# Kernel tuning notes

Hardware: AMD Instinct MI355X
Metric: run time of the kernel (lower is better)

The kernel has to match this reference:

```python
import jax, jax.numpy as jnp
import numpy as np

P = 512
H, W = 256, 256
TANFOVX = 0.5
TANFOVY = 0.5
NEAR = 0.2  # frustum near-plane cull as in 3DGS preprocess
COV_BLUR = 0.3  # low-pass filter added to 2D covariance diagonal (3DGS)
ALPHA_MIN = 1.0 / 255.0
ALPHA_MAX = 0.99


def quat_to_rotmat(q):
    # q: [P,4] normalized (r, x, y, z) -> [P,3,3]
    r, x, y, z = q[:, 0], q[:, 1], q[:, 2], q[:, 3]
    R = jnp.stack([
        1 - 2 * (y * y + z * z), 2 * (x * y - r * z), 2 * (x * z + r * y),
        2 * (x * y + r * z), 1 - 2 * (x * x + z * z), 2 * (y * z - r * x),
        2 * (x * z - r * y), 2 * (y * z + r * x), 1 - 2 * (x * x + y * y),
    ], axis=-1)
    return R.reshape(-1, 3, 3)


def setup_inputs() -> dict:
    key = jax.random.key(0)
    ks = jax.random.split(key, 6)
    # Gaussians in front of a camera at the origin looking down +z.
    xy = jax.random.uniform(ks[0], (P, 2), minval=-2.0, maxval=2.0)
    z = jax.random.uniform(ks[1], (P, 1), minval=2.0, maxval=6.0)
    means3D = jnp.concatenate([xy, z], axis=-1).astype(jnp.float32)
    opacities = jax.random.normal(ks[2], (P, 1), dtype=jnp.float32)  # logits
    scales = (jnp.log(0.05) + 0.3 * jax.random.normal(ks[3], (P, 3))).astype(jnp.float32)  # log-scales
    rotations = jax.random.normal(ks[4], (P, 4), dtype=jnp.float32)  # raw quats
    colors_precomp = jax.random.uniform(ks[5], (P, 3), dtype=jnp.float32)
    viewmatrix = jnp.eye(4, dtype=jnp.float32)
    n, f = NEAR, 100.0
    proj = np.zeros((4, 4), np.float32)
    proj[0, 0] = 1.0 / TANFOVX
    proj[1, 1] = 1.0 / TANFOVY
    proj[2, 2] = f / (f - n)
    proj[2, 3] = -f * n / (f - n)
    proj[3, 2] = 1.0
    projmatrix = jnp.asarray(proj)  # full (proj @ view) since view = I
    campos = jnp.zeros(3, jnp.float32)
    bg = jnp.zeros(3, jnp.float32)
    return dict(means3D=means3D, opacities=opacities, scales=scales,
                rotations=rotations, colors_precomp=colors_precomp,
                viewmatrix=viewmatrix, projmatrix=projmatrix, campos=campos, bg=bg)


def reference(means3D, opacities, scales, rotations, colors_precomp,
              viewmatrix, projmatrix, campos, bg):
    # --- activations applied by the autograd Function forward ---
    opa = jax.nn.sigmoid(opacities[:, 0])                      # [P]
    s = jnp.exp(scales)                                        # [P,3]
    q = rotations / jnp.clip(jnp.linalg.norm(rotations, axis=-1, keepdims=True), 1e-12)
    R = quat_to_rotmat(q)                                      # [P,3,3]
    # 3D covariance: cov = (R S)(R S)^T
    L = R * s[:, None, :]
    cov3D = jnp.einsum('pij,pkj->pik', L, L)                   # [P,3,3]
    # --- camera-space transform ---
    t = means3D @ viewmatrix[:3, :3].T + viewmatrix[:3, 3]     # [P,3]
    tx, ty, tz = t[:, 0], t[:, 1], t[:, 2]
    valid = tz > NEAR
    tzc = jnp.where(valid, tz, 1.0)
    limx, limy = 1.3 * TANFOVX, 1.3 * TANFOVY
    txz = jnp.clip(tx / tzc, -limx, limx) * tzc
    tyz = jnp.clip(ty / tzc, -limy, limy) * tzc
    fx = W / (2.0 * TANFOVX)
    fy = H / (2.0 * TANFOVY)
    # --- EWA splatting: 2D covariance = J W cov3D W^T J^T ---
    zeros = jnp.zeros_like(tzc)
    J = jnp.stack([
        jnp.stack([fx / tzc, zeros, -fx * txz / (tzc * tzc)], axis=-1),
        jnp.stack([zeros, fy / tzc, -fy * tyz / (tzc * tzc)], axis=-1),
    ], axis=-2)                                                # [P,2,3]
    T = jnp.einsum('pij,jk->pik', J, viewmatrix[:3, :3])       # [P,2,3]
    cov2D = jnp.einsum('pij,pjk,plk->pil', T, cov3D, T)        # [P,2,2]
    cov2D = cov2D + COV_BLUR * jnp.eye(2, dtype=cov2D.dtype)
    det = cov2D[:, 0, 0] * cov2D[:, 1, 1] - cov2D[:, 0, 1] ** 2
    det = jnp.where(det == 0.0, 1.0, det)
    conA = cov2D[:, 1, 1] / det
    conB = -cov2D[:, 0, 1] / det
    conC = cov2D[:, 0, 0] / det
    # --- projection to pixel coordinates ---
    ph = jnp.concatenate([means3D, jnp.ones((means3D.shape[0], 1), means3D.dtype)], -1) @ projmatrix.T
    pw = 1.0 / (ph[:, 3] + 1e-7)
    pix_x = ((ph[:, 0] * pw + 1.0) * W - 1.0) * 0.5            # [P]
    pix_y = ((ph[:, 1] * pw + 1.0) * H - 1.0) * 0.5
    # --- global front-to-back depth sort (stand-in for tile binning + per-tile sort) ---
    depth = jnp.where(valid, tz, jnp.inf)
    order = jnp.argsort(depth)
    opa_s = opa[order]
    conA_s, conB_s, conC_s = conA[order], conB[order], conC[order]
    px_s, py_s = pix_x[order], pix_y[order]
    valid_s = valid[order]
    col_s = colors_precomp[order]
    # --- dense alpha compositing over all pixels ---
    xg = jnp.arange(W, dtype=jnp.float32)
    yg = jnp.arange(H, dtype=jnp.float32)
    dx = px_s[:, None, None] - xg[None, None, :]               # [P,1,W]
    dy = py_s[:, None, None] - yg[None, :, None]               # [P,H,1]
    power = (-0.5 * (conA_s[:, None, None] * dx * dx + conC_s[:, None, None] * dy * dy)
             - conB_s[:, None, None] * dx * dy)                # [P,H,W]
    alpha = jnp.minimum(ALPHA_MAX, opa_s[:, None, None] * jnp.exp(power))
    alpha = jnp.where((power > 0.0) | (alpha < ALPHA_MIN) | (~valid_s[:, None, None]), 0.0, alpha)
    Tcum = jnp.cumprod(1.0 - alpha, axis=0)                    # [P,H,W]
    Tprev = jnp.concatenate([jnp.ones((1, H, W), alpha.dtype), Tcum[:-1]], axis=0)
    wgt = alpha * Tprev                                        # per-Gaussian compositing weight
    out_color = jnp.einsum('phw,pc->hwc', wgt, col_s) + Tcum[-1][..., None] * bg  # [H,W,3]
    return out_color
```

## Files before the change

### kernel.cpp

```cpp
#include <hip/hip_runtime.h>
#include <math.h>

#define PCOUNT 512
#define IMG_W 256
#define IMG_H 256
#define TANX 0.5f
#define TANY 0.5f
#define NEARP 0.2f
#define BLUR 0.3f
#define AMIN (1.0f/255.0f)
#define AMAX 0.99f

__global__ __launch_bounds__(256) void fused_raster_kernel(
    const float* __restrict__ means, const float* __restrict__ opac,
    const float* __restrict__ scales, const float* __restrict__ rots,
    const float* __restrict__ cols, const float* __restrict__ vm,
    const float* __restrict__ pm, const float* __restrict__ bg,
    float* __restrict__ out)
{
    __shared__ float s_params[PCOUNT * 12];
    __shared__ float s_depth[PCOUNT];
    __shared__ unsigned short s_order[PCOUNT];
    __shared__ int s_wcnt[4];
    __shared__ int s_base;

    int t = threadIdx.x;
    int wave = t >> 6, lane = t & 63;
    int tileX = blockIdx.x & 15, tileY = blockIdx.x >> 4;
    float tx0 = (float)(tileX << 4), tx1 = tx0 + 15.0f;
    float ty0 = (float)(tileY << 4), ty1 = ty0 + 15.0f;

    if (t == 0) s_base = 0;
    __syncthreads();

    #pragma unroll
    for (int c = 0; c < 2; ++c) {
        int g = c * 256 + t;

        float mx = means[3*g], my = means[3*g+1], mz = means[3*g+2];
        float o = 1.0f / (1.0f + __expf(-opac[g]));
        float sx = __expf(scales[3*g]), sy = __expf(scales[3*g+1]), sz = __expf(scales[3*g+2]);

        float qr = rots[4*g], qx = rots[4*g+1], qy = rots[4*g+2], qz = rots[4*g+3];
        float qn = fmaxf(sqrtf(qr*qr + qx*qx + qy*qy + qz*qz), 1e-12f);
        float qi = 1.0f/qn;
        qr *= qi; qx *= qi; qy *= qi; qz *= qi;

        float R00 = 1.0f-2.0f*(qy*qy+qz*qz), R01 = 2.0f*(qx*qy - qr*qz), R02 = 2.0f*(qx*qz + qr*qy);
        float R10 = 2.0f*(qx*qy + qr*qz), R11 = 1.0f-2.0f*(qx*qx+qz*qz), R12 = 2.0f*(qy*qz - qr*qx);
        float R20 = 2.0f*(qx*qz - qr*qy), R21 = 2.0f*(qy*qz + qr*qx), R22 = 1.0f-2.0f*(qx*qx+qy*qy);

        float s0 = sx*sx, s1 = sy*sy, s2 = sz*sz;
        float c00 = R00*R00*s0 + R01*R01*s1 + R02*R02*s2;
        float c01 = R00*R10*s0 + R01*R11*s1 + R02*R12*s2;
        float c02 = R00*R20*s0 + R01*R21*s1 + R02*R22*s2;
        float c11 = R10*R10*s0 + R11*R11*s1 + R12*R12*s2;
        float c12 = R10*R20*s0 + R11*R21*s1 + R12*R22*s2;
        float c22 = R20*R20*s0 + R21*R21*s1 + R22*R22*s2;

        float tx = vm[0]*mx + vm[1]*my + vm[2]*mz + vm[3];
        float ty = vm[4]*mx + vm[5]*my + vm[6]*mz + vm[7];
        float tz = vm[8]*mx + vm[9]*my + vm[10]*mz + vm[11];
        bool valid = tz > NEARP;
        float tzc = valid ? tz : 1.0f;

        float limx = 1.3f*TANX, limy = 1.3f*TANY;
        float txz = fminf(fmaxf(tx/tzc, -limx), limx)*tzc;
        float tyz = fminf(fmaxf(ty/tzc, -limy), limy)*tzc;

        float fx = (float)IMG_W/(2.0f*TANX), fy = (float)IMG_H/(2.0f*TANY);
        float J00 = fx/tzc, J02 = -fx*txz/(tzc*tzc);
        float J11 = fy/tzc, J12 = -fy*tyz/(tzc*tzc);

        float T00 = J00*vm[0] + J02*vm[8];
        float T01 = J00*vm[1] + J02*vm[9];
        float T02 = J00*vm[2] + J02*vm[10];
        float T10 = J11*vm[4] + J12*vm[8];
        float T11 = J11*vm[5] + J12*vm[9];
        float T12 = J11*vm[6] + J12*vm[10];

        float M00 = T00*c00 + T01*c01 + T02*c02;
        float M01 = T00*c01 + T01*c11 + T02*c12;
        float M02 = T00*c02 + T01*c12 + T02*c22;
        float M10 = T10*c00 + T11*c01 + T12*c02;
        float M11 = T10*c01 + T11*c11 + T12*c12;
        float M12 = T10*c02 + T11*c12 + T12*c22;
        float v00 = M00*T00 + M01*T01 + M02*T02 + BLUR;
        float v01 = M00*T10 + M01*T11 + M02*T12;
        float v11 = M10*T10 + M11*T11 + M12*T12 + BLUR;

        float det = v00*v11 - v01*v01;
        det = (det == 0.0f) ? 1.0f : det;
        float idet = 1.0f/det;
        float conA = v11*idet, conB = -v01*idet, conC = v00*idet;

        float ph0 = pm[0]*mx + pm[1]*my + pm[2]*mz + pm[3];
        float ph1 = pm[4]*mx + pm[5]*my + pm[6]*mz + pm[7];
        float ph3 = pm[12]*mx + pm[13]*my + pm[14]*mz + pm[15];
        float pw = 1.0f/(ph3 + 1e-7f);
        float px = ((ph0*pw + 1.0f)*(float)IMG_W - 1.0f)*0.5f;
        float py = ((ph1*pw + 1.0f)*(float)IMG_H - 1.0f)*0.5f;

        float opa_eff = valid ? o : 0.0f;

        bool hit = false;
        float oa = opa_eff * 255.0f;
        if (oa > 1.0f) {
            float r2 = 2.0f * __logf(oa);
            float dxm = sqrtf(r2 * v00) + 1.0f;
            float dym = sqrtf(r2 * v11) + 1.0f;
            hit = (px - dxm <= tx1) & (px + dxm >= tx0) &
                  (py - dym <= ty1) & (py + dym >= ty0);
        }

        unsigned long long m = __ballot(hit);
        int rnk = __popcll(m & ((1ull << lane) - 1ull));
        if (lane == 0) s_wcnt[wave] = __popcll(m);
        __syncthreads();
        int off = s_base;
        for (int w = 0; w < wave; ++w) off += s_wcnt[w];
        if (hit) {
            int slot = off + rnk;
            float* p = &s_params[slot * 12];
            p[0] = conA; p[1] = conB; p[2] = conC; p[3] = px;
            p[4] = py;   p[5] = opa_eff;
            p[6] = cols[3*g]; p[7] = cols[3*g+1]; p[8] = cols[3*g+2];
            s_depth[slot] = tz;
        }
        __syncthreads();
        if (t == 0) s_base += s_wcnt[0] + s_wcnt[1] + s_wcnt[2] + s_wcnt[3];
        __syncthreads();
    }
    int total = s_base;

    if (t < total) {
        float dk = s_depth[t];
        int rank = 0;
        for (int j = 0; j < total; ++j) {
            float dj = s_depth[j];
            rank += (int)((dj < dk) || (dj == dk && j < t));
        }
        s_order[rank] = (unsigned short)t;
    }
    __syncthreads();

    int lx = t & 15, ly = t >> 4;
    float fxp = tx0 + (float)lx, fyp = ty0 + (float)ly;

    float T = 1.0f, cr = 0.0f, cg = 0.0f, cb = 0.0f;
    for (int i = 0; i < total; ++i) {
        int k = s_order[i];
        const float* p = &s_params[k * 12];
        float4 p0 = *(const float4*)(p);
        float4 p1 = *(const float4*)(p + 4);
        float pb  = p[8];
        float dx = p0.w - fxp;
        float dy = p1.x - fyp;
        float power = -0.5f*(p0.x*dx*dx + p0.z*dy*dy) - p0.y*dx*dy;
        if (power <= 0.0f) {
            float al = p1.y * __expf(power);
            if (al >= AMIN) {
                al = fminf(al, AMAX);
                float w = al * T;
                cr += w * p1.z;
                cg += w * p1.w;
                cb += w * pb;
                T *= (1.0f - al);
            }
        }
    }

    int x = (tileX << 4) + lx, y = (tileY << 4) + ly;
    int o = (y*IMG_W + x)*3;
    out[o+0] = cr + T*bg[0];
    out[o+1] = cg + T*bg[1];
    out[o+2] = cb + T*bg[2];
}

extern "C" void kernel_launch(void* const* d_in, const int* in_sizes, int n_in,
                              void* d_out, int out_size, void* d_ws, size_t ws_size,
                              hipStream_t stream) {
    const float* means  = (const float*)d_in[0];
    const float* opac   = (const float*)d_in[1];
    const float* scales = (const float*)d_in[2];
    const float* rots   = (const float*)d_in[3];
    const float* cols   = (const float*)d_in[4];
    const float* vm     = (const float*)d_in[5];
    const float* pm     = (const float*)d_in[6];
    const float* bg     = (const float*)d_in[8];

    fused_raster_kernel<<<256, 256, 0, stream>>>(
        means, opac, scales, rots, cols, vm, pm, bg, (float*)d_out);
}
```

Measured before the change: 13.24 us.

## Split per-pixel compositing across four depth segments with 1024-thread blocks

Raises the block size to 1024 threads. Each Gaussian is preprocessed by its own thread instead of looping over two chunks, which drops the extra barriers. The depth-sorted list is split into four contiguous segments, and each segment is composited by a separate group of 256 threads. The partial (color, transmittance) results are then combined in order through shared memory. This shortens the serial per-pixel loop, at the cost of losing early-termination benefits, an extra reduction step, and more shared memory per block.

Result: faster. 10.63 us (-19.7%).

```diff
diff --git a/kernel.cpp b/kernel.cpp
--- a/kernel.cpp
+++ b/kernel.cpp
@@ -11,7 +11,7 @@
 #define AMIN (1.0f/255.0f)
 #define AMAX 0.99f
 
-__global__ __launch_bounds__(256) void fused_raster_kernel(
+__global__ __launch_bounds__(1024) void fused_raster_kernel(
     const float* __restrict__ means, const float* __restrict__ opac,
     const float* __restrict__ scales, const float* __restrict__ rots,
     const float* __restrict__ cols, const float* __restrict__ vm,
@@ -21,8 +21,9 @@
     __shared__ float s_params[PCOUNT * 12];
     __shared__ float s_depth[PCOUNT];
     __shared__ unsigned short s_order[PCOUNT];
-    __shared__ int s_wcnt[4];
-    __shared__ int s_base;
+    __shared__ float4 s_part[4][256];
+    __shared__ int s_wcnt[16];
+    __shared__ int s_total;
 
     int t = threadIdx.x;
     int wave = t >> 6, lane = t & 63;
@@ -30,13 +31,10 @@
     float tx0 = (float)(tileX << 4), tx1 = tx0 + 15.0f;
     float ty0 = (float)(tileY << 4), ty1 = ty0 + 15.0f;
 
-    if (t == 0) s_base = 0;
-    __syncthreads();
-
-    #pragma unroll
-    for (int c = 0; c < 2; ++c) {
-        int g = c * 256 + t;
-
+    bool hit = false;
+    float conA = 0, conB = 0, conC = 0, px = 0, py = 0, opa_eff = 0, tz = 0;
+    int g = t;
+    if (t < PCOUNT) {
         float mx = means[3*g], my = means[3*g+1], mz = means[3*g+2];
         float o = 1.0f / (1.0f + __expf(-opac[g]));
         float sx = __expf(scales[3*g]), sy = __expf(scales[3*g+1]), sz = __expf(scales[3*g+2]);
@@ -58,15 +56,15 @@
         float c12 = R10*R20*s0 + R11*R21*s1 + R12*R22*s2;
         float c22 = R20*R20*s0 + R21*R21*s1 + R22*R22*s2;
 
-        float tx = vm[0]*mx + vm[1]*my + vm[2]*mz + vm[3];
-        float ty = vm[4]*mx + vm[5]*my + vm[6]*mz + vm[7];
-        float tz = vm[8]*mx + vm[9]*my + vm[10]*mz + vm[11];
+        float tvx = vm[0]*mx + vm[1]*my + vm[2]*mz + vm[3];
+        float tvy = vm[4]*mx + vm[5]*my + vm[6]*mz + vm[7];
+        tz = vm[8]*mx + vm[9]*my + vm[10]*mz + vm[11];
         bool valid = tz > NEARP;
         float tzc = valid ? tz : 1.0f;
 
         float limx = 1.3f*TANX, limy = 1.3f*TANY;
-        float txz = fminf(fmaxf(tx/tzc, -limx), limx)*tzc;
-        float tyz = fminf(fmaxf(ty/tzc, -limy), limy)*tzc;
+        float txz = fminf(fmaxf(tvx/tzc, -limx), limx)*tzc;
+        float tyz = fminf(fmaxf(tvy/tzc, -limy), limy)*tzc;
 
         float fx = (float)IMG_W/(2.0f*TANX), fy = (float)IMG_H/(2.0f*TANY);
         float J00 = fx/tzc, J02 = -fx*txz/(tzc*tzc);
@@ -92,18 +90,17 @@
         float det = v00*v11 - v01*v01;
         det = (det == 0.0f) ? 1.0f : det;
         float idet = 1.0f/det;
-        float conA = v11*idet, conB = -v01*idet, conC = v00*idet;
+        conA = v11*idet; conB = -v01*idet; conC = v00*idet;
 
         float ph0 = pm[0]*mx + pm[1]*my + pm[2]*mz + pm[3];
         float ph1 = pm[4]*mx + pm[5]*my + pm[6]*mz + pm[7];
         float ph3 = pm[12]*mx + pm[13]*my + pm[14]*mz + pm[15];
         float pw = 1.0f/(ph3 + 1e-7f);
-        float px = ((ph0*pw + 1.0f)*(float)IMG_W - 1.0f)*0.5f;
-        float py = ((ph1*pw + 1.0f)*(float)IMG_H - 1.0f)*0.5f;
-
-        float opa_eff = valid ? o : 0.0f;
-
-        bool hit = false;
+        px = ((ph0*pw + 1.0f)*(float)IMG_W - 1.0f)*0.5f;
+        py = ((ph1*pw + 1.0f)*(float)IMG_H - 1.0f)*0.5f;
+
+        opa_eff = valid ? o : 0.0f;
+
         float oa = opa_eff * 255.0f;
         if (oa > 1.0f) {
             float r2 = 2.0f * __logf(oa);
@@ -112,26 +109,30 @@
             hit = (px - dxm <= tx1) & (px + dxm >= tx0) &
                   (py - dym <= ty1) & (py + dym >= ty0);
         }
-
-        unsigned long long m = __ballot(hit);
-        int rnk = __popcll(m & ((1ull << lane) - 1ull));
-        if (lane == 0) s_wcnt[wave] = __popcll(m);
-        __syncthreads();
-        int off = s_base;
-        for (int w = 0; w < wave; ++w) off += s_wcnt[w];
-        if (hit) {
-            int slot = off + rnk;
-            float* p = &s_params[slot * 12];
-            p[0] = conA; p[1] = conB; p[2] = conC; p[3] = px;
-            p[4] = py;   p[5] = opa_eff;
-            p[6] = cols[3*g]; p[7] = cols[3*g+1]; p[8] = cols[3*g+2];
-            s_depth[slot] = tz;
-        }
-        __syncthreads();
-        if (t == 0) s_base += s_wcnt[0] + s_wcnt[1] + s_wcnt[2] + s_wcnt[3];
-        __syncthreads();
-    }
-    int total = s_base;
+    }
+
+    unsigned long long m = __ballot(hit);
+    int rnk = __popcll(m & ((1ull << lane) - 1ull));
+    if (lane == 0) s_wcnt[wave] = __popcll(m);
+    __syncthreads();
+    int off = 0;
+    for (int w = 0; w < wave; ++w) off += s_wcnt[w];
+    if (hit) {
+        int slot = off + rnk;
+        float* p = &s_params[slot * 12];
+        p[0] = conA; p[1] = conB; p[2] = conC; p[3] = px;
+        p[4] = py;   p[5] = opa_eff;
+        p[6] = cols[3*g]; p[7] = cols[3*g+1]; p[8] = cols[3*g+2];
+        s_depth[slot] = tz;
+    }
+    if (t == 0) {
+        int s = 0;
+        #pragma unroll
+        for (int w = 0; w < 16; ++w) s += s_wcnt[w];
+        s_total = s;
+    }
+    __syncthreads();
+    int total = s_total;
 
     if (t < total) {
         float dk = s_depth[t];
@@ -144,16 +145,21 @@
     }
     __syncthreads();
 
-    int lx = t & 15, ly = t >> 4;
+    int p = t & 255, seg = t >> 8;
+    int lx = p & 15, ly = p >> 4;
     float fxp = tx0 + (float)lx, fyp = ty0 + (float)ly;
 
+    int seglen = (total + 3) >> 2;
+    int i0 = seg * seglen;
+    int i1 = min(i0 + seglen, total);
+
     float T = 1.0f, cr = 0.0f, cg = 0.0f, cb = 0.0f;
-    for (int i = 0; i < total; ++i) {
+    for (int i = i0; i < i1; ++i) {
         int k = s_order[i];
-        const float* p = &s_params[k * 12];
-        float4 p0 = *(const float4*)(p);
-        float4 p1 = *(const float4*)(p + 4);
-        float pb  = p[8];
+        const float* pp = &s_params[k * 12];
+        float4 p0 = *(const float4*)(pp);
+        float4 p1 = *(const float4*)(pp + 4);
+        float pb  = pp[8];
         float dx = p0.w - fxp;
         float dy = p1.x - fyp;
         float power = -0.5f*(p0.x*dx*dx + p0.z*dy*dy) - p0.y*dx*dy;
@@ -169,12 +175,22 @@
             }
         }
     }
-
-    int x = (tileX << 4) + lx, y = (tileY << 4) + ly;
-    int o = (y*IMG_W + x)*3;
-    out[o+0] = cr + T*bg[0];
-    out[o+1] = cg + T*bg[1];
-    out[o+2] = cb + T*bg[2];
+    s_part[seg][p] = make_float4(cr, cg, cb, T);
+    __syncthreads();
+
+    if (t < 256) {
+        float4 r0 = s_part[0][t], r1 = s_part[1][t], r2 = s_part[2][t], r3 = s_part[3][t];
+        float Tt  = r0.w * r1.w * r2.w * r3.w;
+        float ocr = r0.x + r0.w*(r1.x + r1.w*(r2.x + r2.w*r3.x));
+        float ocg = r0.y + r0.w*(r1.y + r1.w*(r2.y + r2.w*r3.y));
+        float ocb = r0.z + r0.w*(r1.z + r1.w*(r2.z + r2.w*r3.z));
+
+        int x = (tileX << 4) + (t & 15), y = (tileY << 4) + (t >> 4);
+        int o = (y*IMG_W + x)*3;
+        out[o+0] = ocr + Tt*bg[0];
+        out[o+1] = ocg + Tt*bg[1];
+        out[o+2] = ocb + Tt*bg[2];
+    }
 }
 
 extern "C" void kernel_launch(void* const* d_in, const int* in_sizes, int n_in,
@@ -189,6 +205,6 @@
     const float* pm     = (const float*)d_in[6];
     const float* bg     = (const float*)d_in[8];
 
-    fused_raster_kernel<<<256, 256, 0, stream>>>(
+    fused_raster_kernel<<<256, 1024, 0, stream>>>(
         means, opac, scales, rots, cols, vm, pm, bg, (float*)d_out);
 }
```
